# Kernel optimization log

Measured on AMD Instinct MI355X. Metric: run time of the kernel, lower is better.

## Reference

```python
import jax, jax.numpy as jnp
import numpy as np

B, T, H = 4, 2048, 1024
N, D = 16, 64  # heads, key_dim (= value_dim)
SCALE = 1.0 / float(D) ** 0.5


def setup_inputs() -> dict:
    key = jax.random.key(0)
    ks = jax.random.split(key, 10)
    s = 0.02
    return {
        "query": jax.random.normal(ks[0], (B, T, H), jnp.float32),
        "value": jax.random.normal(ks[1], (B, T, H), jnp.float32),
        "Wq": jax.random.normal(ks[2], (N * D, H), jnp.float32) * s,
        "bq": jnp.zeros((N * D,), jnp.float32),
        "Wk": jax.random.normal(ks[3], (N * D, H), jnp.float32) * s,
        "bk": jnp.zeros((N * D,), jnp.float32),
        "Wv": jax.random.normal(ks[4], (N * D, H), jnp.float32) * s,
        "bv": jnp.zeros((N * D,), jnp.float32),
        "Wo": jax.random.normal(ks[5], (H, N * D), jnp.float32) * s,
        "bo": jnp.zeros((H,), jnp.float32),
    }


def reference(query, value, Wq, bq, Wk, bk, Wv, bv, Wo, bo):
    key_in = value  # key=None path: key = value
    q = (query @ Wq.T + bq).reshape(B, -1, N, D)   # [B,T,N,D]
    k = (key_in @ Wk.T + bk).reshape(B, -1, N, D)  # [B,S,N,D]
    v = (value @ Wv.T + bv).reshape(B, -1, N, D)   # [B,S,N,D]
    # scores [T,S,B,N], softmax over S (axis=1), scaled dot-product
    scores = jnp.einsum('btnd,bsnd->tsbn', q, k) * SCALE
    attn = jax.nn.softmax(scores, axis=1)
    # output [B,T,N,D]
    out = jnp.einsum('tsbn,bsnd->btnd', attn, v)
    out = out.reshape(B, T, N * D)
    return out @ Wo.T + bo
```

## Files before the change

kernel.cpp:

```cpp
#include <hip/hip_runtime.h>
#include <cstdint>
#include <cstddef>

typedef unsigned short u16;
typedef __bf16 bf16x8 __attribute__((ext_vector_type(8)));
typedef __bf16 bf16x2 __attribute__((ext_vector_type(2)));
typedef float f32x4 __attribute__((ext_vector_type(4)));
typedef float f32x16 __attribute__((ext_vector_type(16)));

#define B_   4
#define T_   2048
#define H_   1024
#define NH_  16
#define DH_  64
#define M_   (B_ * T_)
#define KDIM 1024
#define QSCALE 0.18033688011112042f

#define BM 128
#define BN 128
#define BK 32

__device__ __forceinline__ u16 f2bf(float f) {
    unsigned u = __float_as_uint(f);
    unsigned r = (u + 0x7fffu + ((u >> 16) & 1u)) >> 16;
    return (u16)r;
}

__device__ __forceinline__ unsigned packbf2(float a, float b) {
    bf16x2 v = { (__bf16)a, (__bf16)b };
    return __builtin_bit_cast(unsigned, v);
}

__device__ __forceinline__ float exp2_fast(float x) {
#if __has_builtin(__builtin_amdgcn_exp2f)
    return __builtin_amdgcn_exp2f(x);
#else
    return exp2f(x);
#endif
}

__device__ __forceinline__ void plswap(unsigned &a, unsigned &b) {
#if __has_builtin(__builtin_amdgcn_permlane32_swap)
    auto r = __builtin_amdgcn_permlane32_swap(a, b, false, false);
    a = (unsigned)r[0]; b = (unsigned)r[1];
#else
    int hi = (threadIdx.x & 32);
    unsigned x = (unsigned)__shfl_xor((int)(hi ? b : a), 32);
    unsigned na = hi ? x : a;
    unsigned nb = hi ? b : x;
    a = na; b = nb;
#endif
}

__device__ __forceinline__ void gload16(const void* g, void* l) {
    __builtin_amdgcn_global_load_lds(
        (const __attribute__((address_space(1))) unsigned int*)g,
        (__attribute__((address_space(3))) unsigned int*)l,
        16, 0, 0);
}

__device__ __forceinline__ f32x16 mfma32(bf16x8 a, bf16x8 b, f32x16 c) {
    return __builtin_amdgcn_mfma_f32_32x32x16_bf16(a, b, c, 0, 0, 0);
}

__device__ __forceinline__ void wait_barrier() {
    asm volatile("s_waitcnt vmcnt(0) lgkmcnt(0)\n\ts_barrier" ::: "memory");
}

__global__ __launch_bounds__(256) void f2bf_hex(
    const float* s0, u16* d0, int n0, const float* s1, u16* d1, int n1,
    const float* s2, u16* d2, int n2, const float* s3, u16* d3, int n3,
    const float* s4, u16* d4, int n4j, const float* s5, u16* d5, int n5)
{
    const float* s; u16* d; int n;
    switch (blockIdx.y) {
        case 0: s = s0; d = d0; n = n0; break;
        case 1: s = s1; d = d1; n = n1; break;
        case 2: s = s2; d = d2; n = n2; break;
        case 3: s = s3; d = d3; n = n3; break;
        case 4: s = s4; d = d4; n = n4j; break;
        default: s = s5; d = d5; n = n5; break;
    }
    int i = blockIdx.x * blockDim.x + threadIdx.x;
    int stride = gridDim.x * blockDim.x;
    for (; i < n; i += stride) {
        float4 f = reinterpret_cast<const float4*>(s)[i];
        ushort4 o;
        o.x = f2bf(f.x); o.y = f2bf(f.y); o.z = f2bf(f.z); o.w = f2bf(f.w);
        reinterpret_cast<ushort4*>(d)[i] = o;
    }
}

__device__ __forceinline__ void gemm_core(
    const u16* __restrict__ X, const u16* __restrict__ W,
    const float* __restrict__ bias,
    u16* __restrict__ dst_bf, float* __restrict__ dst_f,
    float scale, int mode, int r0, int c0)
{
    __shared__ u16 lds[17408];
    char* const base = (char*)lds;

    const int tid = threadIdx.x;
    const int wid = tid >> 6;
    const int l15 = tid & 15;
    const int l4  = (tid & 63) >> 4;
    const int wr = wid >> 1, wc = wid & 1;

    const u16* gA = X + (size_t)(r0 + (tid >> 2)) * KDIM + (tid & 3) * 8;
    const u16* gB = W + (size_t)(c0 + (tid >> 2)) * KDIM + (tid & 3) * 8;

    f32x4 acc[4][4];
#pragma unroll
    for (int m = 0; m < 4; ++m)
#pragma unroll
        for (int n = 0; n < 4; ++n) acc[m][n] = (f32x4){0.f, 0.f, 0.f, 0.f};

    const int arow = wr * 64 + l15;
    const int brow = wc * 64 + l15;

#define STAGEG(p, kt) do { \
    const u16* pa_ = gA + (kt) * BK; \
    const u16* pb_ = gB + (kt) * BK; \
    char* dA_ = base + (p) * 16384 + wid * 1024; \
    char* dB_ = dA_ + 8192; \
    gload16(pa_, dA_); gload16(pa_ + 64 * KDIM, dA_ + 4096); \
    gload16(pb_, dB_); gload16(pb_ + 64 * KDIM, dB_ + 4096); } while (0)

    STAGEG(0, 0);
    wait_barrier();

    for (int kt = 0; kt < KDIM / BK; ++kt) {
        if (kt + 1 < KDIM / BK) STAGEG((kt + 1) & 1, kt + 1);
        const char* bufp = base + (kt & 1) * 16384;
        bf16x8 a[4], b[4];
#pragma unroll
        for (int m = 0; m < 4; ++m)
            a[m] = *(const bf16x8*)(bufp + (arow + m * 16) * 64 + l4 * 16);
#pragma unroll
        for (int n = 0; n < 4; ++n)
            b[n] = *(const bf16x8*)(bufp + 8192 + (brow + n * 16) * 64 + l4 * 16);
#pragma unroll
        for (int m = 0; m < 4; ++m)
#pragma unroll
            for (int n = 0; n < 4; ++n)
                acc[m][n] = __builtin_amdgcn_mfma_f32_16x16x32_bf16(a[m], b[n], acc[m][n], 0, 0, 0);
        wait_barrier();
    }
#undef STAGEG

    if (mode == 2) {
#pragma unroll
        for (int m = 0; m < 4; ++m)
#pragma unroll
            for (int n = 0; n < 4; ++n) {
                int cg = c0 + wc * 64 + n * 16 + l15;
                float bv = bias[cg];
                int rg = r0 + wr * 64 + m * 16 + l4 * 4;
#pragma unroll
                for (int j = 0; j < 4; ++j)
                    dst_f[(size_t)(rg + j) * H_ + cg] = acc[m][n][j] + bv;
            }
    } else if (mode == 0) {
        __syncthreads();
        u16 (*ldsR)[136] = (u16(*)[136])lds;
#pragma unroll
        for (int m = 0; m < 4; ++m)
#pragma unroll
            for (int n = 0; n < 4; ++n) {
                int cl = wc * 64 + n * 16 + l15;
                float bv = bias[c0 + cl];
                int rl = wr * 64 + m * 16 + l4 * 4;
#pragma unroll
                for (int j = 0; j < 4; ++j)
                    ldsR[rl + j][cl] = f2bf((acc[m][n][j] + bv) * scale);
            }
        __syncthreads();
        int b2 = r0 >> 11, tb = r0 & (T_ - 1);
#pragma unroll
        for (int it = 0; it < 8; ++it) {
            int id = tid + it * 256;
            int row = id >> 4;
            int ch = id & 15;
            int head = (c0 >> 6) + (ch >> 3);
            int d0 = (ch & 7) * 8;
            uint4 v = *(const uint4*)&ldsR[row][ch * 8];
            *(uint4*)&dst_bf[(((size_t)(b2 * NH_ + head) * T_ + tb + row) << 6) + d0] = v;
        }
    } else {
        __syncthreads();
        u16 (*ldsT)[136] = (u16(*)[136])lds;
#pragma unroll
        for (int m = 0; m < 4; ++m)
#pragma unroll
            for (int n = 0; n < 4; ++n) {
                int cl = wc * 64 + n * 16 + l15;
                float bv = bias[c0 + cl];
                int rl = wr * 64 + m * 16 + l4 * 4;
#pragma unroll
                for (int j = 0; j < 4; ++j)
                    ldsT[cl][rl + j] = f2bf(acc[m][n][j] + bv);
            }
        __syncthreads();
        int b = r0 >> 11, tb = r0 & (T_ - 1);
#pragma unroll
        for (int it = 0; it < 8; ++it) {
            int chunk = tid + it * 256;
            int cl = chunk >> 4;
            int r8 = (chunk & 15) << 3;
            int cg = c0 + cl;
            int head = cg >> 6, d = cg & 63;
            uint4 v = *(const uint4*)&ldsT[cl][r8];
            *(uint4*)&dst_bf[((size_t)((b * NH_ + head) * DH_ + d) * T_) + tb + r8] = v;
        }
    }
}

__global__ __launch_bounds__(256) void gemm_qkv(
    const u16* __restrict__ qbf, const u16* __restrict__ vbf,
    const u16* __restrict__ Wqb, const u16* __restrict__ Wkb, const u16* __restrict__ Wvb,
    const float* __restrict__ bq, const float* __restrict__ bk, const float* __restrict__ bv,
    u16* __restrict__ Qd, u16* __restrict__ Kd, u16* __restrict__ Vtd)
{
    const int orig = blockIdx.y * 24 + blockIdx.x;
    const int swz = (orig & 7) * 192 + (orig >> 3);
    const int bx = swz % 24;
    const int by = swz / 24;
    const int seg = bx >> 3;
    const int r0 = by * BM;
    const int c0 = (bx & 7) * BN;

    if (seg == 0)
        gemm_core(qbf, Wqb, bq, Qd, nullptr, QSCALE, 0, r0, c0);
    else if (seg == 1)
        gemm_core(vbf, Wkb, bk, Kd, nullptr, 1.0f, 0, r0, c0);
    else
        gemm_core(vbf, Wvb, bv, Vtd, nullptr, 1.0f, 1, r0, c0);
}

__global__ __launch_bounds__(256) void gemm_out(
    const u16* __restrict__ AO, const u16* __restrict__ Wob,
    const float* __restrict__ bo, float* __restrict__ out)
{
    const int orig = blockIdx.y * 8 + blockIdx.x;
    const int swz = (orig & 7) * 64 + (orig >> 3);
    const int bx = swz & 7;
    const int by = swz >> 3;
    gemm_core(AO, Wob, bo, nullptr, out, 1.0f, 2, by * BM, bx * BN);
}

#define KVB 64

__global__ __launch_bounds__(256, 2) void attn64(
    const u16* __restrict__ Q, const u16* __restrict__ K,
    const u16* __restrict__ Vt, u16* __restrict__ AO)
{
    __shared__ u16 lds[16384];
    char* const base = (char*)lds;

    const int tid = threadIdx.x;
    const int wid = tid >> 6;
    const int lane = tid & 63;
    const int l31 = lane & 31;
    const int hi = lane >> 5;

    const int orig = blockIdx.y * 8 + blockIdx.x;
    const int swz = (orig & 7) * 64 + (orig >> 3);
    const int bn = swz >> 3;
    const int q0w = (swz & 7) * 256 + wid * 64;
    const int b = bn >> 4, head = bn & 15;

    const u16* Qb = Q + ((size_t)bn * T_ + q0w + l31) * DH_;
    const u16* Kb = K + (size_t)bn * T_ * DH_;
    const u16* Vb = Vt + (size_t)bn * DH_ * T_;

    bf16x8 qfa[4], qfb[4];
#pragma unroll
    for (int c = 0; c < 4; ++c) {
        qfa[c] = *(const bf16x8*)(Qb + c * 16 + hi * 8);
        qfb[c] = *(const bf16x8*)(Qb + 32 * DH_ + c * 16 + hi * 8);
    }

    f32x16 accO00, accO01, accO10, accO11;
#pragma unroll
    for (int r = 0; r < 16; ++r) {
        accO00[r] = 0.f; accO01[r] = 0.f;
        accO10[r] = 0.f; accO11[r] = 0.f;
    }
    float la = 0.f, lb = 0.f;

    const int srow = tid >> 3;
    const int scsw = (tid & 7) ^ (srow & 7);
    const int rowsw = l31 & 7;

    const u16* kSrc = Kb + (size_t)srow * DH_ + scsw * 8;
    const u16* vSrc = Vb + (size_t)srow * T_ + scsw * 8;

#define STAGE(dK, dV) do { \
    gload16(kSrc,            (dK) + tid * 16); \
    gload16(kSrc + 32 * DH_, (dK) + 4096 + tid * 16); \
    gload16(vSrc,            (dV) + tid * 16); \
    gload16(vSrc + 32 * T_,  (dV) + 4096 + tid * 16); \
    kSrc += KVB * DH_; vSrc += KVB; } while (0)

    char* const kb0 = base;
    char* const vb0 = base + 8192;
    char* const kb1 = base + 16384;
    char* const vb1 = base + 24576;

    auto process = [&](const char* kc, const char* vc) {
        f32x16 sA0, sA1, sB0, sB1;
#pragma unroll
        for (int r = 0; r < 16; ++r) { sA0[r] = 0.f; sA1[r] = 0.f; sB0[r] = 0.f; sB1[r] = 0.f; }
        __builtin_amdgcn_s_setprio(1);
#pragma unroll
        for (int c = 0; c < 4; ++c) {
            const int c16 = ((2 * c + hi) ^ rowsw) * 16;
            bf16x8 k0 = *(const bf16x8*)(kc + l31 * 128 + c16);
            bf16x8 k1 = *(const bf16x8*)(kc + 4096 + l31 * 128 + c16);
            sA0 = mfma32(k0, qfa[c], sA0);
            sA1 = mfma32(k1, qfa[c], sA1);
            sB0 = mfma32(k0, qfb[c], sB0);
            sB1 = mfma32(k1, qfb[c], sB1);
        }
        __builtin_amdgcn_s_setprio(0);

#pragma unroll
        for (int r = 0; r < 16; ++r) {
            sA0[r] = exp2_fast(sA0[r]);
            sA1[r] = exp2_fast(sA1[r]);
            sB0[r] = exp2_fast(sB0[r]);
            sB1[r] = exp2_fast(sB1[r]);
        }
        float ta = 0.f, tb2 = 0.f;
#pragma unroll
        for (int r = 0; r < 16; ++r) {
            ta  += sA0[r] + sA1[r];
            tb2 += sB0[r] + sB1[r];
        }
        la += ta; lb += tb2;

        unsigned w0a[8], w1a[8], w0b[8], w1b[8];
#pragma unroll
        for (int k2 = 0; k2 < 8; ++k2) {
            w0a[k2] = packbf2(sA0[2 * k2], sA0[2 * k2 + 1]);
            w1a[k2] = packbf2(sA1[2 * k2], sA1[2 * k2 + 1]);
            w0b[k2] = packbf2(sB0[2 * k2], sB0[2 * k2 + 1]);
            w1b[k2] = packbf2(sB1[2 * k2], sB1[2 * k2 + 1]);
        }
        plswap(w0a[0], w0a[2]); plswap(w0a[1], w0a[3]);
        plswap(w0a[4], w0a[6]); plswap(w0a[5], w0a[7]);
        plswap(w1a[0], w1a[2]); plswap(w1a[1], w1a[3]);
        plswap(w1a[4], w1a[6]); plswap(w1a[5], w1a[7]);
        plswap(w0b[0], w0b[2]); plswap(w0b[1], w0b[3]);
        plswap(w0b[4], w0b[6]); plswap(w0b[5], w0b[7]);
        plswap(w1b[0], w1b[2]); plswap(w1b[1], w1b[3]);
        plswap(w1b[4], w1b[6]); plswap(w1b[5], w1b[7]);

        __builtin_amdgcn_s_setprio(1);
#pragma unroll
        for (int ks = 0; ks < 4; ++ks) {
            union { unsigned w[4]; bf16x8 v; } pa, pb;
            const unsigned* sa_ = (ks < 2) ? w0a : w1a;
            const unsigned* sb_ = (ks < 2) ? w0b : w1b;
            const int o = (ks & 1) * 4;
            pa.w[0] = sa_[o + 0]; pa.w[1] = sa_[o + 1];
            pa.w[2] = sa_[o + 2]; pa.w[3] = sa_[o + 3];
            pb.w[0] = sb_[o + 0]; pb.w[1] = sb_[o + 1];
            pb.w[2] = sb_[o + 2]; pb.w[3] = sb_[o + 3];
            const int c16 = ((2 * ks + hi) ^ rowsw) * 16;
            bf16x8 v0f = *(const bf16x8*)(vc + l31 * 128 + c16);
            bf16x8 v1f = *(const bf16x8*)(vc + 4096 + l31 * 128 + c16);
            accO00 = mfma32(v0f, pa.v, accO00);
            accO01 = mfma32(v1f, pa.v, accO01);
            accO10 = mfma32(v0f, pb.v, accO10);
            accO11 = mfma32(v1f, pb.v, accO11);
        }
        __builtin_amdgcn_s_setprio(0);
    };

    STAGE(kb0, vb0);
    __syncthreads();

    for (int it = 0; it < T_ / KVB; it += 2) {
        STAGE(kb1, vb1);
        process(kb0, vb0);
        __syncthreads();
        if (it + 2 < T_ / KVB) STAGE(kb0, vb0);
        process(kb1, vb1);
        __syncthreads();
    }

    la += __shfl_xor(la, 32);
    lb += __shfl_xor(lb, 32);

    char* myO = base + wid * 8192;
    float inva = 1.f / la;
    float invb = 1.f / lb;
#pragma unroll
    for (int n = 0; n < 2; ++n)
#pragma unroll
        for (int r = 0; r < 16; ++r) {
            int d = n * 32 + (r & 3) + 8 * (r >> 2) + 4 * hi;
            int c16 = (d >> 3) ^ rowsw;
            float va = (n == 0 ? accO00[r] : accO01[r]) * inva;
            float vb2 = (n == 0 ? accO10[r] : accO11[r]) * invb;
            *(u16*)(myO + l31 * 128 + c16 * 16 + (d & 7) * 2) = f2bf(va);
            *(u16*)(myO + (32 + l31) * 128 + c16 * 16 + (d & 7) * 2) = f2bf(vb2);
        }
    asm volatile("s_waitcnt lgkmcnt(0)" ::: "memory");
#pragma unroll
    for (int it = 0; it < 8; ++it) {
        int id = lane + it * 64;
        int row = id >> 3;
        int c = id & 7;
        int c16s = c ^ (row & 7);
        uint4 val = *(const uint4*)(myO + row * 128 + c16s * 16);
        *(uint4*)&AO[(size_t)(b * T_ + q0w + row) * (NH_ * DH_) + head * DH_ + c * 8] = val;
    }
#undef STAGE
}

extern "C" void kernel_launch(void* const* d_in, const int* in_sizes, int n_in,
                              void* d_out, int out_size, void* d_ws, size_t ws_size,
                              hipStream_t stream)
{
    const float* query = (const float*)d_in[0];
    const float* value = (const float*)d_in[1];
    const float* Wq = (const float*)d_in[2];
    const float* bq = (const float*)d_in[3];
    const float* Wk = (const float*)d_in[4];
    const float* bk = (const float*)d_in[5];
    const float* Wv = (const float*)d_in[6];
    const float* bv = (const float*)d_in[7];
    const float* Wo = (const float*)d_in[8];
    const float* bo = (const float*)d_in[9];
    float* out = (float*)d_out;

    u16* ws = (u16*)d_ws;
    const size_t E8M = (size_t)8 << 20;
    u16* qbf = ws;
    u16* vbf = ws + E8M;
    u16* Wqb = ws + 2 * E8M;
    u16* Wkb = Wqb + (1u << 20);
    u16* Wvb = Wkb + (1u << 20);
    u16* Wob = Wvb + (1u << 20);
    u16* Qd  = Wob + (1u << 20);
    u16* Kd  = Qd + E8M;
    u16* Vtd = Kd + E8M;
    u16* AO  = Vtd + E8M;

    const int nBig = (B_ * T_ * H_) / 4;
    const int nW   = (KDIM * KDIM) / 4;
    f2bf_hex<<<dim3(512, 6), 256, 0, stream>>>(
        query, qbf, nBig, value, vbf, nBig,
        Wq, Wqb, nW, Wk, Wkb, nW, Wv, Wvb, nW, Wo, Wob, nW);

    gemm_qkv<<<dim3(24, 64), 256, 0, stream>>>(qbf, vbf, Wqb, Wkb, Wvb,
                                               bq, bk, bv, Qd, Kd, Vtd);

    attn64<<<dim3(8, 64), 256, 0, stream>>>(Qd, Kd, Vtd, AO);

    gemm_out<<<dim3(8, 64), 256, 0, stream>>>(AO, Wob, bo, out);
}
```

Measured before the change: 194.3 us.

## Triple-buffer GEMM LDS staging with two-tile prefetch and partial vmcnt wait

Moves the projection GEMM main loop from double to triple LDS buffering. Loads now run two K-tiles ahead, and each iteration waits with vmcnt(4) instead of draining every outstanding global-to-LDS load. This is meant to hide global load latency behind the MFMA work. The cost is more LDS per block, which may lower the number of resident blocks per CU.

Measured after the change: 183.4 us, median of 2. 1.06x faster.

```diff
diff --git a/kernel.cpp b/kernel.cpp
--- a/kernel.cpp
+++ b/kernel.cpp
@@ -64,10 +64,6 @@
     return __builtin_amdgcn_mfma_f32_32x32x16_bf16(a, b, c, 0, 0, 0);
 }
 
-__device__ __forceinline__ void wait_barrier() {
-    asm volatile("s_waitcnt vmcnt(0) lgkmcnt(0)\n\ts_barrier" ::: "memory");
-}
-
 __global__ __launch_bounds__(256) void f2bf_hex(
     const float* s0, u16* d0, int n0, const float* s1, u16* d1, int n1,
     const float* s2, u16* d2, int n2, const float* s3, u16* d3, int n3,
@@ -98,7 +94,7 @@
     u16* __restrict__ dst_bf, float* __restrict__ dst_f,
     float scale, int mode, int r0, int c0)
 {
-    __shared__ u16 lds[17408];
+    __shared__ u16 lds[24576];
     char* const base = (char*)lds;
 
     const int tid = threadIdx.x;
@@ -127,26 +123,38 @@
     gload16(pa_, dA_); gload16(pa_ + 64 * KDIM, dA_ + 4096); \
     gload16(pb_, dB_); gload16(pb_ + 64 * KDIM, dB_ + 4096); } while (0)
 
+#define COMPUTE(p) do { \
+    const char* bufp = base + (p) * 16384; \
+    bf16x8 a[4], b[4]; \
+    _Pragma("unroll") \
+    for (int m = 0; m < 4; ++m) \
+        a[m] = *(const bf16x8*)(bufp + (arow + m * 16) * 64 + l4 * 16); \
+    _Pragma("unroll") \
+    for (int n = 0; n < 4; ++n) \
+        b[n] = *(const bf16x8*)(bufp + 8192 + (brow + n * 16) * 64 + l4 * 16); \
+    _Pragma("unroll") \
+    for (int m = 0; m < 4; ++m) \
+        _Pragma("unroll") \
+        for (int n = 0; n < 4; ++n) \
+            acc[m][n] = __builtin_amdgcn_mfma_f32_16x16x32_bf16(a[m], b[n], acc[m][n], 0, 0, 0); \
+    } while (0)
+
     STAGEG(0, 0);
-    wait_barrier();
-
-    for (int kt = 0; kt < KDIM / BK; ++kt) {
-        if (kt + 1 < KDIM / BK) STAGEG((kt + 1) & 1, kt + 1);
-        const char* bufp = base + (kt & 1) * 16384;
-        bf16x8 a[4], b[4];
-#pragma unroll
-        for (int m = 0; m < 4; ++m)
-            a[m] = *(const bf16x8*)(bufp + (arow + m * 16) * 64 + l4 * 16);
-#pragma unroll
-        for (int n = 0; n < 4; ++n)
-            b[n] = *(const bf16x8*)(bufp + 8192 + (brow + n * 16) * 64 + l4 * 16);
-#pragma unroll
-        for (int m = 0; m < 4; ++m)
-#pragma unroll
-            for (int n = 0; n < 4; ++n)
-                acc[m][n] = __builtin_amdgcn_mfma_f32_16x16x32_bf16(a[m], b[n], acc[m][n], 0, 0, 0);
-        wait_barrier();
-    }
+    STAGEG(1, 1);
+
+    int p = 0;
+    for (int kt = 0; kt < KDIM / BK - 1; ++kt) {
+        asm volatile("s_waitcnt vmcnt(4) lgkmcnt(0)\n\ts_barrier" ::: "memory");
+        if (kt + 2 < KDIM / BK) {
+            int fp = p + 2; if (fp >= 3) fp -= 3;
+            STAGEG(fp, kt + 2);
+        }
+        COMPUTE(p);
+        ++p; if (p == 3) p = 0;
+    }
+    asm volatile("s_waitcnt vmcnt(0) lgkmcnt(0)\n\ts_barrier" ::: "memory");
+    COMPUTE(p);
+#undef COMPUTE
 #undef STAGEG
 
     if (mode == 2) {
```
